# Performance work log

Hardware: AMD Instinct MI355X
Metric: run time of the kernel (lower is better)

## Reference

```python
import jax, jax.numpy as jnp
import numpy as np

EMBED_DIM = 768
N_HEADS = 12
HEAD_DIM = EMBED_DIM // N_HEADS
B, S = 8, 1024


def setup_inputs() -> dict:
    key = jax.random.key(0)
    ks = jax.random.split(key, 7)
    sc = 1.0 / np.sqrt(HEAD_DIM)
    return {
        "sequences": jax.random.normal(ks[0], (B, S, EMBED_DIM), dtype=jnp.float32),
        # per-head Linear weights stored [H, in, out] (torch Linear is x @ W.T + b;
        # with random init the layout convention is equivalent math)
        "Wq": jax.random.normal(ks[1], (N_HEADS, HEAD_DIM, HEAD_DIM), dtype=jnp.float32) * sc,
        "bq": jax.random.normal(ks[2], (N_HEADS, HEAD_DIM), dtype=jnp.float32) * 0.01,
        "Wk": jax.random.normal(ks[3], (N_HEADS, HEAD_DIM, HEAD_DIM), dtype=jnp.float32) * sc,
        "bk": jax.random.normal(ks[4], (N_HEADS, HEAD_DIM), dtype=jnp.float32) * 0.01,
        "Wv": jax.random.normal(ks[5], (N_HEADS, HEAD_DIM, HEAD_DIM), dtype=jnp.float32) * sc,
        "bv": jax.random.normal(ks[6], (N_HEADS, HEAD_DIM), dtype=jnp.float32) * 0.01,
    }


def reference(sequences, Wq, bq, Wk, bk, Wv, bv):
    b, s, d = sequences.shape
    h, hd = Wq.shape[0], Wq.shape[1]
    x = sequences.reshape(b, s, h, hd)              # split embed dim into heads
    q = jnp.einsum("bshd,hde->bshe", x, Wq) + bq    # per-head linear (block-diag GEMM)
    k = jnp.einsum("bshd,hde->bshe", x, Wk) + bk
    v = jnp.einsum("bshd,hde->bshe", x, Wv) + bv
    # NOTE: original module applies NO 1/sqrt(head_dim) scaling
    logits = jnp.einsum("bshe,bthe->bhst", q, k)    # [B,H,S,S]
    attn = jax.nn.softmax(logits, axis=-1)
    out = jnp.einsum("bhst,bthe->bshe", attn, v)    # [B,S,H,hd]
    return out.reshape(b, s, d)
```

## Files before the change

kernel.cpp:

```cpp
#include <hip/hip_runtime.h>
#include <stdint.h>

#define EMBED 768
#define NH 12
#define HD 64
#define Bsz 8
#define Ssz 1024
#define LOG2E 1.44269504088896f

typedef __attribute__((ext_vector_type(4))) float f32x4;
typedef __attribute__((ext_vector_type(16))) float f32x16;
typedef __attribute__((ext_vector_type(8))) _Float16 f16x8;
typedef __attribute__((ext_vector_type(4))) _Float16 f16x4;
typedef __attribute__((ext_vector_type(2))) _Float16 f16x2;
typedef __attribute__((ext_vector_type(4))) unsigned int u32x4;
typedef __attribute__((ext_vector_type(2))) unsigned int u32x2;

__launch_bounds__(256)
__global__ void qkv_proj(const float* __restrict__ x,
                         const float* __restrict__ Wq, const float* __restrict__ bq,
                         const float* __restrict__ Wk, const float* __restrict__ bk,
                         const float* __restrict__ Wv, const float* __restrict__ bv,
                         _Float16* __restrict__ Qb, _Float16* __restrict__ Kb,
                         _Float16* __restrict__ Vt)
{
    __shared__ _Float16 XT[128 * 72];
    __shared__ _Float16 Wt[3 * 64 * 72];
    __shared__ float Bs[192];

    const int bt = blockIdx.x;
    const int st = bt & 7;
    const int h  = (bt >> 3) % NH;
    const int b  = bt / (8 * NH);
    const int sbase = st * 128;
    const int tid = threadIdx.x;
    const int lane = tid & 63, w = tid >> 6;
    const int l15 = lane & 15, quad = lane >> 4;

    for (int i = 0; i < 8; ++i) {
        int idx = tid + 256 * i;
        int row = idx >> 4;
        int c4  = (idx & 15) * 4;
        const float4 g = *(const float4*)&x[(size_t)(b * Ssz + sbase + row) * EMBED + h * HD + c4];
        f16x4 v; v[0] = (_Float16)g.x; v[1] = (_Float16)g.y; v[2] = (_Float16)g.z; v[3] = (_Float16)g.w;
        *(f16x4*)&XT[row * 72 + c4] = v;
    }
    {
        const float* Ws0[3] = {Wq, Wk, Wv};
        const float* bs0[3] = {bq, bk, bv};
#pragma unroll
        for (int m = 0; m < 3; ++m) {
            const float* W = Ws0[m] + (size_t)h * HD * HD;
            for (int i = 0; i < 4; ++i) {
                int idx = tid + 256 * i;
                int d = idx >> 4, e4 = (idx & 15) * 4;
                float4 g = *(const float4*)&W[d * 64 + e4];
                Wt[m * 4608 + (e4 + 0) * 72 + d] = (_Float16)g.x;
                Wt[m * 4608 + (e4 + 1) * 72 + d] = (_Float16)g.y;
                Wt[m * 4608 + (e4 + 2) * 72 + d] = (_Float16)g.z;
                Wt[m * 4608 + (e4 + 3) * 72 + d] = (_Float16)g.w;
            }
        }
        if (tid < 192) Bs[tid] = bs0[tid >> 6][h * HD + (tid & 63)];
    }
    __syncthreads();

    f16x8 bx[2][2];
    const int nbg0 = w * 2;
#pragma unroll
    for (int nb = 0; nb < 2; ++nb)
#pragma unroll
        for (int kh = 0; kh < 2; ++kh)
            bx[nb][kh] = *(const f16x8*)&XT[((nbg0 + nb) * 16 + l15) * 72 + kh * 32 + quad * 8];
    __syncthreads();

    const size_t qkbase = (size_t)(b * NH + h) * Ssz + sbase;
    const f32x4 zero = {0.f, 0.f, 0.f, 0.f};

#pragma unroll
    for (int m = 0; m < 3; ++m) {
        f32x4 acc[2][4];
#pragma unroll
        for (int nb = 0; nb < 2; ++nb)
#pragma unroll
            for (int eb = 0; eb < 4; ++eb) acc[nb][eb] = zero;
#pragma unroll
        for (int eb = 0; eb < 4; ++eb)
#pragma unroll
            for (int kh = 0; kh < 2; ++kh) {
                f16x8 aw = *(const f16x8*)&Wt[m * 4608 + (eb * 16 + l15) * 72 + kh * 32 + quad * 8];
#pragma unroll
                for (int nb = 0; nb < 2; ++nb)
                    acc[nb][eb] = __builtin_amdgcn_mfma_f32_16x16x32_f16(aw, bx[nb][kh], acc[nb][eb], 0, 0, 0);
            }

        if (m < 2) {
            const float sc = (m == 0) ? LOG2E : 1.0f;
#pragma unroll
            for (int nb = 0; nb < 2; ++nb)
#pragma unroll
                for (int eb = 0; eb < 4; ++eb) {
                    f32x4 bb = *(const f32x4*)&Bs[m * 64 + eb * 16 + quad * 4];
                    f16x4 v;
#pragma unroll
                    for (int r = 0; r < 4; ++r) v[r] = (_Float16)((acc[nb][eb][r] + bb[r]) * sc);
                    *(f16x4*)&XT[((nbg0 + nb) * 16 + l15) * 72 + eb * 16 + quad * 4] = v;
                }
            __syncthreads();
            _Float16* outp = (m == 0) ? Qb : Kb;
            for (int i = 0; i < 4; ++i) {
                int idx = tid + 256 * i;
                int s = idx >> 3, e8 = (idx & 7) * 8;
                *(f16x8*)&outp[(qkbase + s) * HD + e8] = *(const f16x8*)&XT[s * 72 + e8];
            }
            __syncthreads();
        } else {
            _Float16* Vs = XT;
#pragma unroll
            for (int nb = 0; nb < 2; ++nb)
#pragma unroll
                for (int eb = 0; eb < 4; ++eb) {
                    f32x4 bb = *(const f32x4*)&Bs[128 + eb * 16 + quad * 4];
#pragma unroll
                    for (int r = 0; r < 4; ++r)
                        Vs[(eb * 16 + quad * 4 + r) * 136 + (nbg0 + nb) * 16 + l15] =
                            (_Float16)(acc[nb][eb][r] + bb[r]);
                }
            __syncthreads();
            for (int i = 0; i < 4; ++i) {
                int idx = tid + 256 * i;
                int e = idx >> 4, s8 = (idx & 15) * 8;
                *(f16x8*)&Vt[((size_t)(b * NH + h) * 64 + e) * Ssz + sbase + s8] =
                    *(const f16x8*)&Vs[e * 136 + s8];
            }
        }
    }
}

#define KVB 8192
__launch_bounds__(256)
__global__ void attn(const _Float16* __restrict__ Qb, const _Float16* __restrict__ Kb,
                     const _Float16* __restrict__ Vt, float* __restrict__ out)
{
    __shared__ _Float16 KV[2 * KVB];

    const int bt = blockIdx.x;
    const int hh = bt % 96;
    const int qt = bt / 96;
    const int h  = hh % NH;
    const int b  = hh / NH;

    const int tid  = threadIdx.x;
    const int lane = tid & 63, w = tid >> 6;
    const int l31  = lane & 31;
    const int hf   = lane >> 5;

    const size_t bh = (size_t)(b * NH + h);
    const _Float16* Qg = Qb + bh * Ssz * HD;
    const _Float16* Kg = Kb + bh * Ssz * HD;
    const _Float16* Vg = Vt + bh * (size_t)HD * Ssz;

    const int qrow = qt * 128 + w * 32 + l31;
    f16x8 aq[4];
#pragma unroll
    for (int kk = 0; kk < 4; ++kk)
        aq[kk] = *(const f16x8*)&Qg[(size_t)qrow * HD + kk * 16 + hf * 8];

    const int ca = tid, cb = tid + 256;
    const int ra = ca >> 3, ga = (ca & 7) ^ (ra & 7);
    const int rb = cb >> 3, gb = (cb & 7) ^ (rb & 7);
    const _Float16* Ka  = Kg + ra * HD + ga * 8;
    const _Float16* Kb2 = Kg + rb * HD + gb * 8;
    const _Float16* Va  = Vg + (size_t)ra * Ssz + ga * 8;
    const _Float16* Vb  = Vg + (size_t)rb * Ssz + gb * 8;

#define STAGE(buf, kt_) do {                                                            \
    __builtin_amdgcn_global_load_lds(                                                   \
        (const __attribute__((address_space(1))) void*)(Ka + (kt_) * 64 * HD),          \
        (__attribute__((address_space(3))) void*)&KV[(buf) * KVB + ca * 8], 16, 0, 0);  \
    __builtin_amdgcn_global_load_lds(                                                   \
        (const __attribute__((address_space(1))) void*)(Kb2 + (kt_) * 64 * HD),         \
        (__attribute__((address_space(3))) void*)&KV[(buf) * KVB + cb * 8], 16, 0, 0);  \
    __builtin_amdgcn_global_load_lds(                                                   \
        (const __attribute__((address_space(1))) void*)(Va + (kt_) * 64),               \
        (__attribute__((address_space(3))) void*)&KV[(buf) * KVB + 4096 + ca * 8], 16, 0, 0); \
    __builtin_amdgcn_global_load_lds(                                                   \
        (const __attribute__((address_space(1))) void*)(Vb + (kt_) * 64),               \
        (__attribute__((address_space(3))) void*)&KV[(buf) * KVB + 4096 + cb * 8], 16, 0, 0); \
} while (0)

    STAGE(0, 0);

    f32x16 o0, o1;
#pragma unroll
    for (int i = 0; i < 16; ++i) { o0[i] = 0.f; o1[i] = 0.f; }
    float m_run = -INFINITY, l_run = 0.f;

    const int rsw = l31 * 64;
    const int sx  = (l31 & 7) << 3;
    const int ch  = hf * 8;

    __asm__ __volatile__("s_waitcnt vmcnt(0)" ::: "memory");
    __syncthreads();

    for (int kt = 0; kt < 16; ++kt) {
        const int cur = kt & 1;
        if (kt < 15) STAGE(cur ^ 1, kt + 1);

        const _Float16* Ksb = &KV[cur * KVB];
        const _Float16* Vsb = &KV[cur * KVB + 4096];

        f32x16 st0, st1;
#pragma unroll
        for (int i = 0; i < 16; ++i) { st0[i] = 0.f; st1[i] = 0.f; }
        __builtin_amdgcn_s_setprio(1);
#pragma unroll
        for (int kk = 0; kk < 4; ++kk) {
            const int col = (kk * 16 + ch) ^ sx;
            f16x8 ak0 = *(const f16x8*)&Ksb[rsw + col];
            f16x8 ak1 = *(const f16x8*)&Ksb[2048 + rsw + col];
            st0 = __builtin_amdgcn_mfma_f32_32x32x16_f16(ak0, aq[kk], st0, 0, 0, 0);
            st1 = __builtin_amdgcn_mfma_f32_32x32x16_f16(ak1, aq[kk], st1, 0, 0, 0);
        }
        __builtin_amdgcn_s_setprio(0);

        float mt = st0[0];
#pragma unroll
        for (int i = 1; i < 16; ++i) mt = fmaxf(mt, st0[i]);
#pragma unroll
        for (int i = 0; i < 16; ++i) mt = fmaxf(mt, st1[i]);
        mt = fmaxf(mt, __shfl_xor(mt, 32, 64));

        if (__any(mt > m_run + 8.f)) {
            float mn = fmaxf(m_run, mt);
            float al = __builtin_amdgcn_exp2f(m_run - mn);
            m_run = mn;
            l_run *= al;
#pragma unroll
            for (int i = 0; i < 16; ++i) { o0[i] *= al; o1[i] *= al; }
        }

#pragma unroll
        for (int i = 0; i < 16; ++i) st0[i] = __builtin_amdgcn_exp2f(st0[i] - m_run);
#pragma unroll
        for (int i = 0; i < 16; ++i) st1[i] = __builtin_amdgcn_exp2f(st1[i] - m_run);

        float a0 = 0.f, a1 = 0.f, a2 = 0.f, a3 = 0.f;
#pragma unroll
        for (int i = 0; i < 16; i += 4) {
            a0 += st0[i]; a1 += st0[i+1]; a2 += st0[i+2]; a3 += st0[i+3];
            a0 += st1[i]; a1 += st1[i+1]; a2 += st1[i+2]; a3 += st1[i+3];
        }
        l_run += (a0 + a1) + (a2 + a3);

        __builtin_amdgcn_s_setprio(1);
#pragma unroll
        for (int kk = 0; kk < 4; ++kk) {
            const f32x16& pp = (kk < 2) ? st0 : st1;
            const int c = 8 * (kk & 1);
            unsigned X0 = __builtin_bit_cast(unsigned, __builtin_amdgcn_cvt_pkrtz(pp[c+0], pp[c+1]));
            unsigned X1 = __builtin_bit_cast(unsigned, __builtin_amdgcn_cvt_pkrtz(pp[c+2], pp[c+3]));
            unsigned Y0 = __builtin_bit_cast(unsigned, __builtin_amdgcn_cvt_pkrtz(pp[c+4], pp[c+5]));
            unsigned Y1 = __builtin_bit_cast(unsigned, __builtin_amdgcn_cvt_pkrtz(pp[c+6], pp[c+7]));
            u32x2 r02 = __builtin_amdgcn_permlane32_swap(X0, Y0, 0, 0);
            u32x2 r13 = __builtin_amdgcn_permlane32_swap(X1, Y1, 0, 0);
            u32x4 du = {r02[0], r13[0], r02[1], r13[1]};
            f16x8 bp = __builtin_bit_cast(f16x8, du);
            const int col = (kk * 16 + ch) ^ sx;
            f16x8 av0 = *(const f16x8*)&Vsb[rsw + col];
            f16x8 av1 = *(const f16x8*)&Vsb[2048 + rsw + col];
            o0 = __builtin_amdgcn_mfma_f32_32x32x16_f16(av0, bp, o0, 0, 0, 0);
            o1 = __builtin_amdgcn_mfma_f32_32x32x16_f16(av1, bp, o1, 0, 0, 0);
        }
        __builtin_amdgcn_s_setprio(0);

        __asm__ __volatile__("s_waitcnt vmcnt(0)" ::: "memory");
        __syncthreads();
    }

    l_run += __shfl_xor(l_run, 32, 64);
    const float inv = 1.f / l_run;
    float* op = &out[((size_t)b * Ssz + qrow) * EMBED + h * HD];
#pragma unroll
    for (int r1 = 0; r1 < 4; ++r1) {
        f32x4 v0, v1;
#pragma unroll
        for (int r0 = 0; r0 < 4; ++r0) {
            v0[r0] = o0[4 * r1 + r0] * inv;
            v1[r0] = o1[4 * r1 + r0] * inv;
        }
        *(f32x4*)&op[r1 * 8 + hf * 4]      = v0;
        *(f32x4*)&op[32 + r1 * 8 + hf * 4] = v1;
    }
#undef STAGE
}

extern "C" void kernel_launch(void* const* d_in, const int* in_sizes, int n_in,
                              void* d_out, int out_size, void* d_ws, size_t ws_size,
                              hipStream_t stream) {
    const float* x  = (const float*)d_in[0];
    const float* Wq = (const float*)d_in[1];
    const float* bq = (const float*)d_in[2];
    const float* Wk = (const float*)d_in[3];
    const float* bk = (const float*)d_in[4];
    const float* Wv = (const float*)d_in[5];
    const float* bv = (const float*)d_in[6];

    _Float16* Qb = (_Float16*)d_ws;
    _Float16* Kb = Qb + (size_t)Bsz * NH * Ssz * HD;
    _Float16* Vt = Kb + (size_t)Bsz * NH * Ssz * HD;

    qkv_proj<<<dim3(Bsz * NH * 8), dim3(256), 0, stream>>>(x, Wq, bq, Wk, bk, Wv, bv, Qb, Kb, Vt);
    attn<<<dim3(Bsz * NH * 8), dim3(256), 0, stream>>>(Qb, Kb, Vt, (float*)d_out);
}
```

Measured before the change: 132.7 us.

## Software-pipeline QK^T one tile ahead with triple-buffered KV staging

```diff
diff --git a/kernel.cpp b/kernel.cpp
--- a/kernel.cpp
+++ b/kernel.cpp
@@ -138,11 +138,11 @@
 }
 
 #define KVB 8192
-__launch_bounds__(256)
+__launch_bounds__(256, 2)
 __global__ void attn(const _Float16* __restrict__ Qb, const _Float16* __restrict__ Kb,
                      const _Float16* __restrict__ Vt, float* __restrict__ out)
 {
-    __shared__ _Float16 KV[2 * KVB];
+    __shared__ _Float16 KV[3 * KVB];
 
     const int bt = blockIdx.x;
     const int hh = bt % 96;
@@ -189,46 +189,66 @@
         (__attribute__((address_space(3))) void*)&KV[(buf) * KVB + 4096 + cb * 8], 16, 0, 0); \
 } while (0)
 
-    STAGE(0, 0);
-
-    f32x16 o0, o1;
-#pragma unroll
-    for (int i = 0; i < 16; ++i) { o0[i] = 0.f; o1[i] = 0.f; }
-    float m_run = -INFINITY, l_run = 0.f;
-
     const int rsw = l31 * 64;
     const int sx  = (l31 & 7) << 3;
     const int ch  = hf * 8;
 
+#define QKT(d0, d1, bufi) do {                                                   \
+    const _Float16* Ksb_ = &KV[(bufi) * KVB];                                    \
+    _Pragma("unroll")                                                            \
+    for (int i_ = 0; i_ < 16; ++i_) { d0[i_] = 0.f; d1[i_] = 0.f; }              \
+    __builtin_amdgcn_s_setprio(1);                                               \
+    _Pragma("unroll")                                                            \
+    for (int kk_ = 0; kk_ < 4; ++kk_) {                                          \
+        const int col_ = (kk_ * 16 + ch) ^ sx;                                   \
+        f16x8 ak0_ = *(const f16x8*)&Ksb_[rsw + col_];                           \
+        f16x8 ak1_ = *(const f16x8*)&Ksb_[2048 + rsw + col_];                    \
+        d0 = __builtin_amdgcn_mfma_f32_32x32x16_f16(ak0_, aq[kk_], d0, 0, 0, 0); \
+        d1 = __builtin_amdgcn_mfma_f32_32x32x16_f16(ak1_, aq[kk_], d1, 0, 0, 0); \
+    }                                                                            \
+    __builtin_amdgcn_s_setprio(0);                                               \
+} while (0)
+
+    STAGE(0, 0);
+
+    f32x16 o0, o1;
+#pragma unroll
+    for (int i = 0; i < 16; ++i) { o0[i] = 0.f; o1[i] = 0.f; }
+    float m_run = -INFINITY, l_run = 0.f;
+
     __asm__ __volatile__("s_waitcnt vmcnt(0)" ::: "memory");
     __syncthreads();
 
+    STAGE(1, 1);
+    f32x16 sA0, sA1, sB0, sB1;
+    QKT(sA0, sA1, 0);
+
+    __asm__ __volatile__("s_waitcnt vmcnt(0)" ::: "memory");
+    __syncthreads();
+
+#pragma unroll
     for (int kt = 0; kt < 16; ++kt) {
-        const int cur = kt & 1;
-        if (kt < 15) STAGE(cur ^ 1, kt + 1);
-
-        const _Float16* Ksb = &KV[cur * KVB];
-        const _Float16* Vsb = &KV[cur * KVB + 4096];
-
-        f32x16 st0, st1;
-#pragma unroll
-        for (int i = 0; i < 16; ++i) { st0[i] = 0.f; st1[i] = 0.f; }
-        __builtin_amdgcn_s_setprio(1);
-#pragma unroll
-        for (int kk = 0; kk < 4; ++kk) {
-            const int col = (kk * 16 + ch) ^ sx;
-            f16x8 ak0 = *(const f16x8*)&Ksb[rsw + col];
-            f16x8 ak1 = *(const f16x8*)&Ksb[2048 + rsw + col];
-            st0 = __builtin_amdgcn_mfma_f32_32x32x16_f16(ak0, aq[kk], st0, 0, 0, 0);
-            st1 = __builtin_amdgcn_mfma_f32_32x32x16_f16(ak1, aq[kk], st1, 0, 0, 0);
-        }
-        __builtin_amdgcn_s_setprio(0);
-
-        float mt = st0[0];
-#pragma unroll
-        for (int i = 1; i < 16; ++i) mt = fmaxf(mt, st0[i]);
-#pragma unroll
-        for (int i = 0; i < 16; ++i) mt = fmaxf(mt, st1[i]);
+        const int bc = kt % 3;
+        const int bn = (kt + 1) % 3;
+        const int bs = (kt + 2) % 3;
+
+        if (kt < 14) STAGE(bs, kt + 2);
+
+        if (kt < 15) {
+            if (kt & 1) QKT(sA0, sA1, bn);
+            else        QKT(sB0, sB1, bn);
+        }
+
+        f32x16& c0 = (kt & 1) ? sB0 : sA0;
+        f32x16& c1 = (kt & 1) ? sB1 : sA1;
+
+        float m8[8];
+#pragma unroll
+        for (int i = 0; i < 8; ++i)
+            m8[i] = fmaxf(fmaxf(c0[i], c0[i + 8]), fmaxf(c1[i], c1[i + 8]));
+        float m4a = fmaxf(m8[0], m8[4]), m4b = fmaxf(m8[1], m8[5]);
+        float m4c = fmaxf(m8[2], m8[6]), m4d = fmaxf(m8[3], m8[7]);
+        float mt = fmaxf(fmaxf(m4a, m4b), fmaxf(m4c, m4d));
         mt = fmaxf(mt, __shfl_xor(mt, 32, 64));
 
         if (__any(mt > m_run + 8.f)) {
@@ -241,22 +261,23 @@
         }
 
 #pragma unroll
-        for (int i = 0; i < 16; ++i) st0[i] = __builtin_amdgcn_exp2f(st0[i] - m_run);
-#pragma unroll
-        for (int i = 0; i < 16; ++i) st1[i] = __builtin_amdgcn_exp2f(st1[i] - m_run);
+        for (int i = 0; i < 16; ++i) c0[i] = __builtin_amdgcn_exp2f(c0[i] - m_run);
+#pragma unroll
+        for (int i = 0; i < 16; ++i) c1[i] = __builtin_amdgcn_exp2f(c1[i] - m_run);
 
         float a0 = 0.f, a1 = 0.f, a2 = 0.f, a3 = 0.f;
 #pragma unroll
         for (int i = 0; i < 16; i += 4) {
-            a0 += st0[i]; a1 += st0[i+1]; a2 += st0[i+2]; a3 += st0[i+3];
-            a0 += st1[i]; a1 += st1[i+1]; a2 += st1[i+2]; a3 += st1[i+3];
+            a0 += c0[i]; a1 += c0[i+1]; a2 += c0[i+2]; a3 += c0[i+3];
+            a0 += c1[i]; a1 += c1[i+1]; a2 += c1[i+2]; a3 += c1[i+3];
         }
         l_run += (a0 + a1) + (a2 + a3);
 
+        const _Float16* Vsb = &KV[bc * KVB + 4096];
         __builtin_amdgcn_s_setprio(1);
 #pragma unroll
         for (int kk = 0; kk < 4; ++kk) {
-            const f32x16& pp = (kk < 2) ? st0 : st1;
+            const f32x16& pp = (kk < 2) ? c0 : c1;
             const int c = 8 * (kk & 1);
             unsigned X0 = __builtin_bit_cast(unsigned, __builtin_amdgcn_cvt_pkrtz(pp[c+0], pp[c+1]));
             unsigned X1 = __builtin_bit_cast(unsigned, __builtin_amdgcn_cvt_pkrtz(pp[c+2], pp[c+3]));
@@ -274,8 +295,10 @@
         }
         __builtin_amdgcn_s_setprio(0);
 
-        __asm__ __volatile__("s_waitcnt vmcnt(0)" ::: "memory");
-        __syncthreads();
+        if (kt < 15) {
+            __asm__ __volatile__("s_waitcnt vmcnt(0)" ::: "memory");
+            __syncthreads();
+        }
     }
 
     l_run += __shfl_xor(l_run, 32, 64);
@@ -293,6 +316,7 @@
         *(f32x4*)&op[32 + r1 * 8 + hf * 4] = v1;
     }
 #undef STAGE
+#undef QKT
 }
 
 extern "C" void kernel_launch(void* const* d_in, const int* in_sizes, int n_in,
```

New measurement: 129.6 us. -2.4%, faster.

## Triple-buffer K/V staging and fold softmax row sums into fdot2 on packed f16

Applied to the files above, without the earlier changes.

```diff
diff --git a/kernel.cpp b/kernel.cpp
--- a/kernel.cpp
+++ b/kernel.cpp
@@ -13,6 +13,7 @@
 typedef __attribute__((ext_vector_type(8))) _Float16 f16x8;
 typedef __attribute__((ext_vector_type(4))) _Float16 f16x4;
 typedef __attribute__((ext_vector_type(2))) _Float16 f16x2;
+typedef __attribute__((ext_vector_type(2))) __fp16 h16x2;
 typedef __attribute__((ext_vector_type(4))) unsigned int u32x4;
 typedef __attribute__((ext_vector_type(2))) unsigned int u32x2;
 
@@ -138,11 +139,11 @@
 }
 
 #define KVB 8192
-__launch_bounds__(256)
+__launch_bounds__(256, 2)
 __global__ void attn(const _Float16* __restrict__ Qb, const _Float16* __restrict__ Kb,
                      const _Float16* __restrict__ Vt, float* __restrict__ out)
 {
-    __shared__ _Float16 KV[2 * KVB];
+    __shared__ _Float16 KV[3 * KVB];
 
     const int bt = blockIdx.x;
     const int hh = bt % 96;
@@ -189,33 +190,44 @@
         (__attribute__((address_space(3))) void*)&KV[(buf) * KVB + 4096 + cb * 8], 16, 0, 0); \
 } while (0)
 
-    STAGE(0, 0);
-
-    f32x16 o0, o1;
-#pragma unroll
-    for (int i = 0; i < 16; ++i) { o0[i] = 0.f; o1[i] = 0.f; }
-    float m_run = -INFINITY, l_run = 0.f;
-
     const int rsw = l31 * 64;
     const int sx  = (l31 & 7) << 3;
     const int ch  = hf * 8;
 
-    __asm__ __volatile__("s_waitcnt vmcnt(0)" ::: "memory");
+    STAGE(0, 0);
+    STAGE(1, 1);
+
+    f32x16 o0, o1, zero16;
+#pragma unroll
+    for (int i = 0; i < 16; ++i) { o0[i] = 0.f; o1[i] = 0.f; zero16[i] = 0.f; }
+    float m_run = -INFINITY;
+    float la = 0.f, lb = 0.f, lc = 0.f, ld = 0.f;
+    h16x2 ones2; ones2[0] = (__fp16)1.0f; ones2[1] = (__fp16)1.0f;
+
+    __asm__ __volatile__("s_waitcnt vmcnt(4)" ::: "memory");
     __syncthreads();
 
+#pragma unroll
     for (int kt = 0; kt < 16; ++kt) {
-        const int cur = kt & 1;
-        if (kt < 15) STAGE(cur ^ 1, kt + 1);
-
-        const _Float16* Ksb = &KV[cur * KVB];
-        const _Float16* Vsb = &KV[cur * KVB + 4096];
+        const int bc = kt % 3;
+        const int bs = (kt + 2) % 3;
+
+        if (kt < 14) STAGE(bs, kt + 2);
+
+        const _Float16* Ksb = &KV[bc * KVB];
+        const _Float16* Vsb = &KV[bc * KVB + 4096];
 
         f32x16 st0, st1;
-#pragma unroll
-        for (int i = 0; i < 16; ++i) { st0[i] = 0.f; st1[i] = 0.f; }
         __builtin_amdgcn_s_setprio(1);
-#pragma unroll
-        for (int kk = 0; kk < 4; ++kk) {
+        {
+            const int col0 = ch ^ sx;
+            f16x8 ak0 = *(const f16x8*)&Ksb[rsw + col0];
+            f16x8 ak1 = *(const f16x8*)&Ksb[2048 + rsw + col0];
+            st0 = __builtin_amdgcn_mfma_f32_32x32x16_f16(ak0, aq[0], zero16, 0, 0, 0);
+            st1 = __builtin_amdgcn_mfma_f32_32x32x16_f16(ak1, aq[0], zero16, 0, 0, 0);
+        }
+#pragma unroll
+        for (int kk = 1; kk < 4; ++kk) {
             const int col = (kk * 16 + ch) ^ sx;
             f16x8 ak0 = *(const f16x8*)&Ksb[rsw + col];
             f16x8 ak1 = *(const f16x8*)&Ksb[2048 + rsw + col];
@@ -224,18 +236,20 @@
         }
         __builtin_amdgcn_s_setprio(0);
 
-        float mt = st0[0];
-#pragma unroll
-        for (int i = 1; i < 16; ++i) mt = fmaxf(mt, st0[i]);
-#pragma unroll
-        for (int i = 0; i < 16; ++i) mt = fmaxf(mt, st1[i]);
+        float m8[8];
+#pragma unroll
+        for (int i = 0; i < 8; ++i)
+            m8[i] = fmaxf(fmaxf(st0[i], st0[i + 8]), fmaxf(st1[i], st1[i + 8]));
+        float m4a = fmaxf(m8[0], m8[4]), m4b = fmaxf(m8[1], m8[5]);
+        float m4c = fmaxf(m8[2], m8[6]), m4d = fmaxf(m8[3], m8[7]);
+        float mt = fmaxf(fmaxf(m4a, m4b), fmaxf(m4c, m4d));
         mt = fmaxf(mt, __shfl_xor(mt, 32, 64));
 
         if (__any(mt > m_run + 8.f)) {
             float mn = fmaxf(m_run, mt);
             float al = __builtin_amdgcn_exp2f(m_run - mn);
             m_run = mn;
-            l_run *= al;
+            la *= al; lb *= al; lc *= al; ld *= al;
 #pragma unroll
             for (int i = 0; i < 16; ++i) { o0[i] *= al; o1[i] *= al; }
         }
@@ -244,24 +258,24 @@
         for (int i = 0; i < 16; ++i) st0[i] = __builtin_amdgcn_exp2f(st0[i] - m_run);
 #pragma unroll
         for (int i = 0; i < 16; ++i) st1[i] = __builtin_amdgcn_exp2f(st1[i] - m_run);
-
-        float a0 = 0.f, a1 = 0.f, a2 = 0.f, a3 = 0.f;
-#pragma unroll
-        for (int i = 0; i < 16; i += 4) {
-            a0 += st0[i]; a1 += st0[i+1]; a2 += st0[i+2]; a3 += st0[i+3];
-            a0 += st1[i]; a1 += st1[i+1]; a2 += st1[i+2]; a3 += st1[i+3];
-        }
-        l_run += (a0 + a1) + (a2 + a3);
 
         __builtin_amdgcn_s_setprio(1);
 #pragma unroll
         for (int kk = 0; kk < 4; ++kk) {
             const f32x16& pp = (kk < 2) ? st0 : st1;
             const int c = 8 * (kk & 1);
-            unsigned X0 = __builtin_bit_cast(unsigned, __builtin_amdgcn_cvt_pkrtz(pp[c+0], pp[c+1]));
-            unsigned X1 = __builtin_bit_cast(unsigned, __builtin_amdgcn_cvt_pkrtz(pp[c+2], pp[c+3]));
-            unsigned Y0 = __builtin_bit_cast(unsigned, __builtin_amdgcn_cvt_pkrtz(pp[c+4], pp[c+5]));
-            unsigned Y1 = __builtin_bit_cast(unsigned, __builtin_amdgcn_cvt_pkrtz(pp[c+6], pp[c+7]));
+            h16x2 x0h = __builtin_amdgcn_cvt_pkrtz(pp[c+0], pp[c+1]);
+            h16x2 x1h = __builtin_amdgcn_cvt_pkrtz(pp[c+2], pp[c+3]);
+            h16x2 y0h = __builtin_amdgcn_cvt_pkrtz(pp[c+4], pp[c+5]);
+            h16x2 y1h = __builtin_amdgcn_cvt_pkrtz(pp[c+6], pp[c+7]);
+            la = __builtin_amdgcn_fdot2(x0h, ones2, la, false);
+            lb = __builtin_amdgcn_fdot2(x1h, ones2, lb, false);
+            lc = __builtin_amdgcn_fdot2(y0h, ones2, lc, false);
+            ld = __builtin_amdgcn_fdot2(y1h, ones2, ld, false);
+            unsigned X0 = __builtin_bit_cast(unsigned, x0h);
+            unsigned X1 = __builtin_bit_cast(unsigned, x1h);
+            unsigned Y0 = __builtin_bit_cast(unsigned, y0h);
+            unsigned Y1 = __builtin_bit_cast(unsigned, y1h);
             u32x2 r02 = __builtin_amdgcn_permlane32_swap(X0, Y0, 0, 0);
             u32x2 r13 = __builtin_amdgcn_permlane32_swap(X1, Y1, 0, 0);
             u32x4 du = {r02[0], r13[0], r02[1], r13[1]};
@@ -274,10 +288,16 @@
         }
         __builtin_amdgcn_s_setprio(0);
 
-        __asm__ __volatile__("s_waitcnt vmcnt(0)" ::: "memory");
-        __syncthreads();
-    }
-
+        if (kt < 14) {
+            __asm__ __volatile__("s_waitcnt vmcnt(4)" ::: "memory");
+            __syncthreads();
+        } else if (kt < 15) {
+            __asm__ __volatile__("s_waitcnt vmcnt(0)" ::: "memory");
+            __syncthreads();
+        }
+    }
+
+    float l_run = (la + lb) + (lc + ld);
     l_run += __shfl_xor(l_run, 32, 64);
     const float inv = 1.f / l_run;
     float* op = &out[((size_t)b * Ssz + qrow) * EMBED + h * HD];
```

Result: no change. 130.1 us (-1.9%).
